# Performance work log

Hardware: AMD Instinct MI355X
Metric: run time of the kernel (lower is better)

The kernel has to match this reference:

```python
import jax, jax.numpy as jnp
import numpy as np

N_OBJ = 4096
IN_DIM = 1024
OUT_DIM = 1024
H = OUT_DIM // 2  # per-direction hidden, BidirectionalTreeLSTM uses out_dim//2
L = 2             # num_layer


def _build_tree(n):
    # balanced binary heap tree: node i has children 2i+1, 2i+2
    left = np.array([2 * i + 1 if 2 * i + 1 < n else -1 for i in range(n)], np.int32)
    right = np.array([2 * i + 2 if 2 * i + 2 < n else -1 for i in range(n)], np.int32)
    parent = np.full(n, -1, np.int32)
    for i in range(n):
        if left[i] >= 0:
            parent[left[i]] = i
        if right[i] >= 0:
            parent[right[i]] = i
    post, stack = [], [(0, False)]
    while stack:
        node, seen = stack.pop()
        if node < 0:
            continue
        if seen:
            post.append(node)
        else:
            stack.append((node, True))
            stack.append((int(right[node]), False))
            stack.append((int(left[node]), False))
    pre, stack = [], [0]
    while stack:
        node = stack.pop()
        if node < 0:
            continue
        pre.append(node)
        stack.append(int(right[node]))
        stack.append(int(left[node]))
    pad = lambda a: np.where(a < 0, n, a).astype(np.int32)  # slot n = zeros (no child/parent)
    return (np.array(post, np.int32), np.array(pre, np.int32),
            pad(left), pad(right), pad(parent))


def setup_inputs() -> dict:
    key = jax.random.key(0)
    ks = jax.random.split(key, 8)
    post, pre, left, right, parent = _build_tree(N_OBJ)

    def w(k, shape, fan_in):
        return jax.random.normal(k, shape, jnp.float32) * np.float32(1.0 / np.sqrt(fan_in))

    # bias init per the torch module: forget-gate blocks get constants, rest zero
    fw_bl = np.zeros((L, 6 * H), np.float32); fw_bl[:, 2 * H:4 * H] = 0.5
    fw_br = fw_bl.copy()
    bw_bh = np.zeros((L, 5 * H), np.float32); bw_bh[:, 2 * H:3 * H] = 1.0

    return {
        "features": jax.random.normal(ks[0], (N_OBJ, IN_DIM), jnp.float32),
        "fw_Wp": w(ks[1], (L, H, IN_DIM), IN_DIM),
        "fw_bp": jnp.zeros((L, H), jnp.float32),
        "fw_Wx": w(ks[2], (L, 6 * H, IN_DIM), IN_DIM),
        "fw_bx": jnp.zeros((L, 6 * H), jnp.float32),
        "fw_Wl": w(ks[3], (L, 6 * H, H), H),
        "fw_bl": jnp.asarray(fw_bl),
        "fw_Wr": w(ks[4], (L, 6 * H, H), H),
        "fw_br": jnp.asarray(fw_br),
        "bw_Wp": w(ks[5], (L, H, IN_DIM), IN_DIM),
        "bw_bp": jnp.zeros((L, H), jnp.float32),
        "bw_Wx": w(ks[6], (L, 5 * H, IN_DIM), IN_DIM),
        "bw_bx": jnp.zeros((L, 5 * H), jnp.float32),
        "bw_Wh": w(ks[7], (L, 5 * H, H), H),
        "bw_bh": jnp.asarray(bw_bh),
        "post_order": jnp.asarray(post),
        "pre_order": jnp.asarray(pre),
        "left_child": jnp.asarray(left),
        "right_child": jnp.asarray(right),
        "parent": jnp.asarray(parent),
    }


def _tree_leaves_to_root(feats, Wp, bp, Wx, bx, Wl, bl, Wr, br,
                         post_order, left_child, right_child):
    n = feats.shape[0]
    h = bp.shape[0]
    px = feats @ Wp.T + bp   # [n, h]   -- self path
    x2 = feats @ Wx.T + bx   # [n, 6h]  -- gate input, batched once

    def step(carry, idx):
        cbuf, hbuf = carry   # [n+1, h]; row n is permanent zero slot for missing children
        lc = left_child[idx]
        rc = right_child[idx]
        g = x2[idx] + hbuf[lc] @ Wl.T + bl + hbuf[rc] @ Wr.T + br
        i, o, fl, fr, u, r = jnp.split(g, 6)
        i = jax.nn.sigmoid(i); o = jax.nn.sigmoid(o)
        fl = jax.nn.sigmoid(fl); fr = jax.nn.sigmoid(fr)
        u = jnp.tanh(u); r = jax.nn.sigmoid(r)
        c = i * u + fl * cbuf[lc] + fr * cbuf[rc]
        hc = o * jnp.tanh(c)
        hf = r * hc + (1.0 - r) * px[idx]   # highway mix
        return (cbuf.at[idx].set(c), hbuf.at[idx].set(hf)), None

    init = (jnp.zeros((n + 1, h), feats.dtype), jnp.zeros((n + 1, h), feats.dtype))
    (_, hbuf), _ = jax.lax.scan(step, init, post_order)
    return hbuf[:n]


def _tree_root_to_leaves(feats, Wp, bp, Wx, bx, Wh, bh, pre_order, parent):
    n = feats.shape[0]
    h = bp.shape[0]
    px = feats @ Wp.T + bp   # [n, h]
    x2 = feats @ Wx.T + bx   # [n, 5h]

    def step(carry, idx):
        cbuf, hbuf = carry
        p = parent[idx]      # root maps to zero slot n -> iofuh(0) == bias, as in torch
        g = x2[idx] + hbuf[p] @ Wh.T + bh
        i, o, f, u, r = jnp.split(g, 5)
        i = jax.nn.sigmoid(i); o = jax.nn.sigmoid(o)
        f = jax.nn.sigmoid(f); u = jnp.tanh(u); r = jax.nn.sigmoid(r)
        c = i * u + f * cbuf[p]
        hc = o * jnp.tanh(c)
        hf = r * hc + (1.0 - r) * px[idx]
        return (cbuf.at[idx].set(c), hbuf.at[idx].set(hf)), None

    init = (jnp.zeros((n + 1, h), feats.dtype), jnp.zeros((n + 1, h), feats.dtype))
    (_, hbuf), _ = jax.lax.scan(step, init, pre_order)
    return hbuf[:n]


def reference(features, fw_Wp, fw_bp, fw_Wx, fw_bx, fw_Wl, fw_bl, fw_Wr, fw_br,
              bw_Wp, bw_bp, bw_Wx, bw_bx, bw_Wh, bw_bh,
              post_order, pre_order, left_child, right_child, parent):
    feats = features
    for l in range(L):  # MultiLayer_BTreeLSTM: stacked bidirectional layers
        h_fwd = _tree_leaves_to_root(feats, fw_Wp[l], fw_bp[l], fw_Wx[l], fw_bx[l],
                                     fw_Wl[l], fw_bl[l], fw_Wr[l], fw_br[l],
                                     post_order, left_child, right_child)
        h_bwd = _tree_root_to_leaves(feats, bw_Wp[l], bw_bp[l], bw_Wx[l], bw_bx[l],
                                     bw_Wh[l], bw_bh[l], pre_order, parent)
        feats = jnp.concatenate([h_fwd, h_bwd], axis=1)  # [n, out_dim]
    return feats
```

## Files before the change

kernel.cpp:

```cpp
#include <hip/hip_runtime.h>
#include <cstdint>
#include <cstddef>


#define HDIM 512
#define ZROW 4096
#define NCAT 6656

typedef _Float16 f16;
typedef f16   f16x8 __attribute__((ext_vector_type(8)));
typedef float f32x4 __attribute__((ext_vector_type(4)));

__device__ __forceinline__ float sigm(float x) { return 1.0f / (1.0f + expf(-x)); }

__device__ __forceinline__ void glds16(const f16* g, f16* l)
{
    __builtin_amdgcn_global_load_lds(
        (const __attribute__((address_space(1))) void*)g,
        (__attribute__((address_space(3))) void*)l,
        16, 0, 0);
}

#define VM4()   asm volatile("s_waitcnt vmcnt(4)" ::: "memory")
#define VM0()   asm volatile("s_waitcnt vmcnt(0)" ::: "memory")
#define BAR()   __builtin_amdgcn_s_barrier()
#define SP1()   __builtin_amdgcn_s_setprio(1)
#define SP0()   __builtin_amdgcn_s_setprio(0)

__device__ __forceinline__ void cvt8s(const float* __restrict__ s, f16* __restrict__ d)
{
    float4 v0 = ((const float4*)s)[0];
    float4 v1 = ((const float4*)s)[1];
    f16x8 o;
    o[0] = (f16)v0.x; o[1] = (f16)v0.y; o[2] = (f16)v0.z; o[3] = (f16)v0.w;
    o[4] = (f16)v1.x; o[5] = (f16)v1.y; o[6] = (f16)v1.z; o[7] = (f16)v1.w;
    *(f16x8*)d = o;
}

__global__ __launch_bounds__(256) void cvt16(
    const float* __restrict__ s, f16* __restrict__ d, int n8)
{
    int i = blockIdx.x * 256 + threadIdx.x;
    if (i >= n8) return;
    cvt8s(s + (size_t)i * 8, d + (size_t)i * 8);
}

__global__ __launch_bounds__(256) void prep_layer(
    const float* __restrict__ fWp, const float* __restrict__ fWx,
    const float* __restrict__ bWp, const float* __restrict__ bWx,
    const float* __restrict__ fWl, const float* __restrict__ fWr,
    const float* __restrict__ bWh,
    const float* __restrict__ fbp, const float* __restrict__ fbx,
    const float* __restrict__ bbp, const float* __restrict__ bbx,
    f16* __restrict__ Wcat, f16* __restrict__ Wlr, f16* __restrict__ Wh,
    float* __restrict__ biascat)
{
    const int bid = blockIdx.x;
    const int t   = threadIdx.x;
    if (bid < 256) {
        int i = bid * 256 + t;
        cvt8s(fWp + (size_t)i * 8, Wcat + (size_t)i * 8);
    } else if (bid < 1792) {
        int i = (bid - 256) * 256 + t;
        cvt8s(fWx + (size_t)i * 8, Wcat + (size_t)512 * 1024 + (size_t)i * 8);
    } else if (bid < 2048) {
        int i = (bid - 1792) * 256 + t;
        cvt8s(bWp + (size_t)i * 8, Wcat + (size_t)3584 * 1024 + (size_t)i * 8);
    } else if (bid < 3328) {
        int i = (bid - 2048) * 256 + t;
        cvt8s(bWx + (size_t)i * 8, Wcat + (size_t)4096 * 1024 + (size_t)i * 8);
    } else if (bid < 4864) {
        int i = (bid - 3328) * 256 + t;
        int col8 = (i * 8) & 1023;
        int row  = (i * 8) >> 10;
        const float* s = (col8 < HDIM) ? (fWl + (size_t)row * HDIM + col8)
                                       : (fWr + (size_t)row * HDIM + col8 - HDIM);
        int np = (row & 511) * 6 + (row >> 9);
        cvt8s(s, Wlr + (size_t)np * 1024 + col8);
    } else if (bid < 5504) {
        int i = (bid - 4864) * 256 + t;
        int col8 = (i * 8) & 511;
        int row  = (i * 8) >> 9;
        int np = (row & 511) * 5 + (row >> 9);
        cvt8s(bWh + (size_t)row * HDIM + col8, Wh + (size_t)np * HDIM + col8);
    } else {
        int i = (bid - 5504) * 256 + t;
        if (i >= NCAT) return;
        float v;
        if (i < 512) v = fbp[i];
        else if (i < 3584) v = fbx[i - 512];
        else if (i < 4096) v = bbp[i - 3584];
        else v = bbx[i - 4096];
        biascat[i] = v;
    }
}

__global__ void zero_slots(f16* H, float* cbf, float* cbb)
{
    int t = threadIdx.x;
    H[(size_t)ZROW * 1024 + t] = (f16)0.0f;
    if (t < HDIM) {
        cbf[(size_t)ZROW * HDIM + t] = 0.0f;
        cbb[(size_t)ZROW * HDIM + t] = 0.0f;
    }
}

__global__ __launch_bounds__(512) void mm_pre8(
    const f16* __restrict__ A, const f16* __restrict__ W,
    const float* __restrict__ bias, f16* __restrict__ C, int N, int K)
{
    __shared__ __align__(16) f16 lds[2][2][16384];
    const int t   = threadIdx.x;
    const int L   = t & 63;
    const int wid = t >> 6;
    const int wr  = wid >> 2;
    const int wc  = wid & 3;
    const int fr  = L & 15;
    const int fq  = L >> 4;
    const int srow = t >> 3;
    const int cs   = (((t & 7) ^ (srow & 7)) << 3);
    const int vrow = ((srow >> 5) << 6) + (srow & 31);
    const int bB0  = (srow >= 32) ? 2048 : 0;
    const f16* Ag = A + (size_t)(blockIdx.y * 256) * K + cs;
    const f16* Bg = W + (size_t)(blockIdx.x * 256) * K + cs;
    const int xa0 = ((fq)     ^ (fr & 7)) << 3;
    const int xa1 = ((4 + fq) ^ (fr & 7)) << 3;

#define STG_A(nb, T, u)                                                      \
    do {                                                                     \
        glds16(Ag + (size_t)(srow + (u) * 64) * K + (T) * 64,                \
               &lds[nb][0][(u) * 4096 + t * 8]);                             \
        glds16(Ag + (size_t)(srow + (u) * 64 + 128) * K + (T) * 64,          \
               &lds[nb][0][(u) * 4096 + 8192 + t * 8]);                      \
    } while (0)
#define STG_B(nb, T, v)                                                      \
    do {                                                                     \
        glds16(Bg + (size_t)(vrow + (v) * 32) * K + (T) * 64,                \
               &lds[nb][1][(v) * 2048 + bB0 + t * 8]);                       \
        glds16(Bg + (size_t)(vrow + (v) * 32 + 128) * K + (T) * 64,          \
               &lds[nb][1][(v) * 2048 + bB0 + 8192 + t * 8]);                \
    } while (0)

    f32x4 acc[8][4] = {};
    f16x8 a0f[4][2], a1f[4][2], b0f[2][2], b1f[2][2];

#define LDA(AF, Ar, mh)                                                            \
    do {                                                                           \
        _Pragma("unroll") for (int i2 = 0; i2 < 4; ++i2) {                         \
            AF[i2][0] = *(const f16x8*)((Ar) + ((mh) * 64 + i2 * 16) * 64 + xa0);  \
            AF[i2][1] = *(const f16x8*)((Ar) + ((mh) * 64 + i2 * 16) * 64 + xa1);  \
        }                                                                          \
    } while (0)
#define LDB(BF, Br, nh)                                                            \
    do {                                                                           \
        _Pragma("unroll") for (int j2 = 0; j2 < 2; ++j2) {                         \
            BF[j2][0] = *(const f16x8*)((Br) + ((nh) * 32 + j2 * 16) * 64 + xa0);  \
            BF[j2][1] = *(const f16x8*)((Br) + ((nh) * 32 + j2 * 16) * 64 + xa1);  \
        }                                                                          \
    } while (0)
#define MF(AF, BF, mh, nh)                                                         \
    do {                                                                           \
        _Pragma("unroll") for (int ks = 0; ks < 2; ++ks)                           \
        _Pragma("unroll") for (int i2 = 0; i2 < 4; ++i2)                           \
        _Pragma("unroll") for (int j2 = 0; j2 < 2; ++j2)                           \
            acc[(mh) * 4 + i2][(nh) * 2 + j2] =                                    \
                __builtin_amdgcn_mfma_f32_16x16x32_f16(                            \
                    AF[i2][ks], BF[j2][ks],                                        \
                    acc[(mh) * 4 + i2][(nh) * 2 + j2], 0, 0, 0);                   \
    } while (0)

    const int NT = K >> 6;
    STG_A(0, 0, 0); STG_B(0, 0, 0); STG_B(0, 0, 1); STG_A(0, 0, 1);
    VM0();
    BAR();

    for (int T = 0; T < NT; ++T) {
        const int cb = T & 1, nb = cb ^ 1;
        const bool pf = (T + 1 < NT);
        const f16* Ar = &lds[cb][0][(wr * 128 + fr) * 64];
        const f16* Br = &lds[cb][1][(wc * 64 + fr) * 64];
        LDA(a0f, Ar, 0); LDB(b0f, Br, 0);
        if (pf) STG_A(nb, T + 1, 0);
        VM4(); BAR();
        SP1(); MF(a0f, b0f, 0, 0); SP0();
        LDB(b1f, Br, 1);
        if (pf) STG_B(nb, T + 1, 0);
        VM4(); BAR();
        SP1(); MF(a0f, b1f, 0, 1); SP0();
        LDA(a1f, Ar, 1);
        if (pf) STG_B(nb, T + 1, 1);
        VM4(); BAR();
        SP1(); MF(a1f, b1f, 1, 1); SP0();
        if (pf) STG_A(nb, T + 1, 1);
        VM4(); BAR();
        SP1(); MF(a1f, b0f, 1, 0); SP0();
    }
#undef STG_A
#undef STG_B
#undef LDA
#undef LDB
#undef MF

    const int gr0 = blockIdx.y * 256 + wr * 128 + fq * 4;
    const int gc0 = blockIdx.x * 256 + wc * 64 + fr;
#pragma unroll
    for (int j = 0; j < 4; ++j) {
        const int gc = gc0 + j * 16;
        const float bj = bias[gc];
#pragma unroll
        for (int i = 0; i < 8; ++i) {
            const int gr = gr0 + i * 16;
#pragma unroll
            for (int rr = 0; rr < 4; ++rr)
                C[(size_t)(gr + rr) * N + gc] = (f16)(acc[i][j][rr] + bj);
        }
    }
}

__global__ __launch_bounds__(256) void stage_fused(
    const f16* __restrict__ Wlr, const f16* __restrict__ Wh,
    f16* H, const f16* __restrict__ PX,
    const int* __restrict__ lc, const int* __restrict__ rc,
    const int* __restrict__ par,
    int fbase, int fm, int bbase, int bm,
    float* __restrict__ cbf, float* __restrict__ cbb,
    float* out32,
    const float* __restrict__ bl, const float* __restrict__ br,
    const float* __restrict__ bh)
{
    __shared__ __align__(16) char smem[57344];
    f16*   Ab0 = (f16*)smem;
    f16*   Bb0 = (f16*)(smem + 32768);
    float* Sg  = (float*)smem;

    const int t   = threadIdx.x;
    const int L   = t & 63;
    const int w   = t >> 6;
    const int fr  = L & 15;
    const int fq  = L >> 4;
    const int rch = L >> 3;
    const int cs  = (((L & 7) ^ rch) << 3);
    const int fsw = (fr & 7) << 3;
    const int nfB = ((fm + 127) >> 7) * 32;

    if ((int)blockIdx.x < nfB) {
        const int by = blockIdx.x >> 5;
        const int bx = blockIdx.x & 31;
        const int wm = (w & 1) << 6;
        const int wn = (w >> 1) * 48;

        const f16* aLo[4]; const f16* aHi[4];
#pragma unroll
        for (int cc = 0; cc < 4; ++cc) {
            int g  = by * 128 + (w * 4 + cc) * 8 + rch;
            int n1 = ZROW, n2 = ZROW;
            if (g < fm) { n1 = lc[fbase + g]; n2 = rc[fbase + g]; }
            aLo[cc] = H + (size_t)n1 * 1024 + cs;
            aHi[cc] = H + (size_t)n2 * 1024 + cs - HDIM;
        }
        const f16* bsrc[3];
#pragma unroll
        for (int cc = 0; cc < 3; ++cc)
            bsrc[cc] = Wlr + (size_t)(bx * 96 + (w * 3 + cc) * 8 + rch) * 1024 + cs;

        f32x4 acc[4][3] = {};
#define STGF(sel, k0)                                                        \
        do {                                                                 \
            const bool hiK = (k0) >= HDIM;                                   \
            _Pragma("unroll")                                                \
            for (int cc = 0; cc < 4; ++cc)                                   \
                glds16((hiK ? aHi[cc] : aLo[cc]) + (k0),                     \
                       Ab0 + (sel) * 8192 + (w * 4 + cc) * 512 + L * 8);     \
            _Pragma("unroll")                                                \
            for (int cc = 0; cc < 3; ++cc)                                   \
                glds16(bsrc[cc] + (k0),                                      \
                       Bb0 + (sel) * 6144 + (w * 3 + cc) * 512 + L * 8);     \
        } while (0)

        STGF(0, 0);
        __syncthreads();
        int cur = 0;
        for (int tt = 0; tt < 16; ++tt) {
            if (tt + 1 < 16) STGF(cur ^ 1, (tt + 1) * 64);
            const f16* Ac = Ab0 + cur * 8192;
            const f16* Bc = Bb0 + cur * 6144;
            f16x8 af[4][2], bg[3][2];
#pragma unroll
            for (int i = 0; i < 4; ++i)
#pragma unroll
                for (int ks = 0; ks < 2; ++ks)
                    af[i][ks] = *(const f16x8*)(Ac + (wm + i * 16 + fr) * 64
                                + ((((ks * 4 + fq) << 3) ^ fsw)));
#pragma unroll
            for (int j = 0; j < 3; ++j)
#pragma unroll
                for (int ks = 0; ks < 2; ++ks)
                    bg[j][ks] = *(const f16x8*)(Bc + (wn + j * 16 + fr) * 64
                                + ((((ks * 4 + fq) << 3) ^ fsw)));
#pragma unroll
            for (int ks = 0; ks < 2; ++ks)
#pragma unroll
                for (int i = 0; i < 4; ++i)
#pragma unroll
                    for (int j = 0; j < 3; ++j)
                        acc[i][j] = __builtin_amdgcn_mfma_f32_16x16x32_f16(
                            af[i][ks], bg[j][ks], acc[i][j], 0, 0, 0);
            __syncthreads();
            cur ^= 1;
        }
#undef STGF
#pragma unroll
        for (int i = 0; i < 4; ++i)
#pragma unroll
            for (int j = 0; j < 3; ++j)
#pragma unroll
                for (int rr = 0; rr < 4; ++rr)
                    Sg[(wm + i * 16 + fq * 4 + rr) * 100 + wn + j * 16 + fr]
                        = acc[i][j][rr];
        __syncthreads();
        const int rmax = fm - by * 128;
        const int j0 = bx * 16;
        for (int cc = 0; cc < 8; ++cc) {
            int cell = t + cc * 256;
            int r = cell >> 4, j = cell & 15;
            if (r >= rmax) break;
            int node = fbase + by * 128 + r;
            int jj = j0 + j;
            const f16* pxr = PX + (size_t)node * NCAT;
            float g[6];
#pragma unroll
            for (int q = 0; q < 6; ++q)
                g[q] = (float)pxr[HDIM + q * HDIM + jj] + bl[q * HDIM + jj]
                     + br[q * HDIM + jj] + Sg[r * 100 + j * 6 + q];
            int lcn = lc[node], rcn = rc[node];
            float clv = cbf[(size_t)lcn * HDIM + jj];
            float crv = cbf[(size_t)rcn * HDIM + jj];
            float i_ = sigm(g[0]), o_ = sigm(g[1]), fl_ = sigm(g[2]), fr_ = sigm(g[3]);
            float u_ = tanhf(g[4]), r_ = sigm(g[5]);
            float c  = i_ * u_ + fl_ * clv + fr_ * crv;
            float hc = o_ * tanhf(c);
            float px = (float)pxr[jj];
            float hf = r_ * hc + (1.0f - r_) * px;
            cbf[(size_t)node * HDIM + jj] = c;
            H[(size_t)node * 1024 + jj] = (f16)hf;
            if (out32) out32[(size_t)node * 1024 + jj] = hf;
        }
    } else {
        const int b2 = blockIdx.x - nfB;
        const int by = b2 >> 5;
        const int bx = b2 & 31;
        const int wm = w * 32;

        const f16* asrc[4];
#pragma unroll
        for (int cc = 0; cc < 4; ++cc) {
            int g = by * 128 + (w * 4 + cc) * 8 + rch;
            int n1 = ZROW;
            if (g < bm) n1 = par[bbase + g];
            asrc[cc] = H + (size_t)n1 * 1024 + HDIM + cs;
        }
        const f16* bsrc[3];
        int nbch[3];
#pragma unroll
        for (int cc = 0; cc < 3; ++cc) {
            int ch = w * 3 + cc;
            nbch[cc] = ch;
            bsrc[cc] = Wh + (size_t)(bx * 80 + ch * 8 + rch) * HDIM + cs;
        }

        f32x4 acc[2][5] = {};
#define STGB(sel, k0)                                                        \
        do {                                                                 \
            _Pragma("unroll")                                                \
            for (int cc = 0; cc < 4; ++cc)                                   \
                glds16(asrc[cc] + (k0),                                      \
                       Ab0 + (sel) * 8192 + (w * 4 + cc) * 512 + L * 8);     \
            _Pragma("unroll")                                                \
            for (int cc = 0; cc < 3; ++cc)                                   \
                if (nbch[cc] < 10)                                           \
                    glds16(bsrc[cc] + (k0),                                  \
                           Bb0 + (sel) * 5120 + nbch[cc] * 512 + L * 8);     \
        } while (0)

        STGB(0, 0);
        __syncthreads();
        int cur = 0;
        for (int tt = 0; tt < 8; ++tt) {
            if (tt + 1 < 8) STGB(cur ^ 1, (tt + 1) * 64);
            const f16* Ac = Ab0 + cur * 8192;
            const f16* Bc = Bb0 + cur * 5120;
            f16x8 af[2][2], bg[5][2];
#pragma unroll
            for (int i = 0; i < 2; ++i)
#pragma unroll
                for (int ks = 0; ks < 2; ++ks)
                    af[i][ks] = *(const f16x8*)(Ac + (wm + i * 16 + fr) * 64
                                + ((((ks * 4 + fq) << 3) ^ fsw)));
#pragma unroll
            for (int j = 0; j < 5; ++j)
#pragma unroll
                for (int ks = 0; ks < 2; ++ks)
                    bg[j][ks] = *(const f16x8*)(Bc + ((j) * 16 + fr) * 64
                                + ((((ks * 4 + fq) << 3) ^ fsw)));
#pragma unroll
            for (int ks = 0; ks < 2; ++ks)
#pragma unroll
                for (int i = 0; i < 2; ++i)
#pragma unroll
                    for (int j = 0; j < 5; ++j)
                        acc[i][j] = __builtin_amdgcn_mfma_f32_16x16x32_f16(
                            af[i][ks], bg[j][ks], acc[i][j], 0, 0, 0);
            __syncthreads();
            cur ^= 1;
        }
#undef STGB
#pragma unroll
        for (int i = 0; i < 2; ++i)
#pragma unroll
            for (int j = 0; j < 5; ++j)
#pragma unroll
                for (int rr = 0; rr < 4; ++rr)
                    Sg[(wm + i * 16 + fq * 4 + rr) * 84 + j * 16 + fr]
                        = acc[i][j][rr];
        __syncthreads();
        const int rmax = bm - by * 128;
        const int j0 = bx * 16;
        for (int cc = 0; cc < 8; ++cc) {
            int cell = t + cc * 256;
            int r = cell >> 4, j = cell & 15;
            if (r >= rmax) break;
            int node = bbase + by * 128 + r;
            int jj = j0 + j;
            const f16* pxr = PX + (size_t)node * NCAT;
            float g[5];
#pragma unroll
            for (int q = 0; q < 5; ++q)
                g[q] = (float)pxr[4096 + q * HDIM + jj] + bh[q * HDIM + jj]
                     + Sg[r * 84 + j * 5 + q];
            int p = par[node];
            float cp = cbb[(size_t)p * HDIM + jj];
            float i_ = sigm(g[0]), o_ = sigm(g[1]), f_ = sigm(g[2]);
            float u_ = tanhf(g[3]), r_ = sigm(g[4]);
            float c  = i_ * u_ + f_ * cp;
            float hc = o_ * tanhf(c);
            float px = (float)pxr[3584 + jj];
            float hf = r_ * hc + (1.0f - r_) * px;
            cbb[(size_t)node * HDIM + jj] = c;
            H[(size_t)node * 1024 + HDIM + jj] = (f16)hf;
            if (out32) out32[(size_t)node * 1024 + HDIM + jj] = hf;
        }
    }
}

__global__ __launch_bounds__(256) void elem_merged(
    const f16* __restrict__ PX,
    int fbase, int fm, int bbase, int bm,
    const int* __restrict__ lc, const int* __restrict__ rc,
    const int* __restrict__ par,
    float* __restrict__ cbf, float* __restrict__ cbb,
    f16* __restrict__ H, float* __restrict__ out32,
    const float* __restrict__ bl, const float* __restrict__ br,
    const float* __restrict__ bh)
{
    int t = blockIdx.x * 256 + threadIdx.x;
    const int fvec = fm * 64;
    if (t < fvec) {
        int row = t >> 6, j8 = (t & 63) << 3;
        int node = fbase + row;
        const f16* pxr = PX + (size_t)node * NCAT;
        float g[6][8];
#pragma unroll
        for (int q = 0; q < 6; ++q) {
            f16x8 pv = *(const f16x8*)(pxr + HDIM + q * HDIM + j8);
            const float* blp = bl + q * HDIM + j8;
            const float* brp = br + q * HDIM + j8;
#pragma unroll
            for (int e = 0; e < 8; ++e)
                g[q][e] = (float)pv[e] + blp[e] + brp[e];
        }
        int lcn = lc[node], rcn = rc[node];
        const float* clp = cbf + (size_t)lcn * HDIM + j8;
        const float* crp = cbf + (size_t)rcn * HDIM + j8;
        f32x4 cl0 = *(const f32x4*)clp, cl1 = *(const f32x4*)(clp + 4);
        f32x4 cr0 = *(const f32x4*)crp, cr1 = *(const f32x4*)(crp + 4);
        f16x8 pxv = *(const f16x8*)(pxr + j8);
        f32x4 co0, co1;
        f16x8 hv;
        f32x4 ho0, ho1;
#pragma unroll
        for (int e = 0; e < 8; ++e) {
            float clv = (e < 4) ? cl0[e & 3] : cl1[e & 3];
            float crv = (e < 4) ? cr0[e & 3] : cr1[e & 3];
            float i_ = sigm(g[0][e]), o_ = sigm(g[1][e]);
            float fl_ = sigm(g[2][e]), fr_ = sigm(g[3][e]);
            float u_ = tanhf(g[4][e]), r_ = sigm(g[5][e]);
            float c  = i_ * u_ + fl_ * clv + fr_ * crv;
            float hc = o_ * tanhf(c);
            float hf = r_ * hc + (1.0f - r_) * (float)pxv[e];
            if (e < 4) { co0[e & 3] = c; ho0[e & 3] = hf; }
            else       { co1[e & 3] = c; ho1[e & 3] = hf; }
            hv[e] = (f16)hf;
        }
        float* cdst = cbf + (size_t)node * HDIM + j8;
        *(f32x4*)cdst = co0; *(f32x4*)(cdst + 4) = co1;
        *(f16x8*)(H + (size_t)node * 1024 + j8) = hv;
        if (out32) {
            float* od = out32 + (size_t)node * 1024 + j8;
            *(f32x4*)od = ho0; *(f32x4*)(od + 4) = ho1;
        }
    } else {
        int t2 = t - fvec;
        if (t2 >= bm * 64) return;
        int row = t2 >> 6, j8 = (t2 & 63) << 3;
        int node = bbase + row;
        const f16* pxr = PX + (size_t)node * NCAT;
        float g[5][8];
#pragma unroll
        for (int q = 0; q < 5; ++q) {
            f16x8 pv = *(const f16x8*)(pxr + 4096 + q * HDIM + j8);
            const float* bhp = bh + q * HDIM + j8;
#pragma unroll
            for (int e = 0; e < 8; ++e)
                g[q][e] = (float)pv[e] + bhp[e];
        }
        int p = par[node];
        const float* cpp = cbb + (size_t)p * HDIM + j8;
        f32x4 cp0 = *(const f32x4*)cpp, cp1 = *(const f32x4*)(cpp + 4);
        f16x8 pxv = *(const f16x8*)(pxr + 3584 + j8);
        f32x4 co0, co1;
        f16x8 hv;
        f32x4 ho0, ho1;
#pragma unroll
        for (int e = 0; e < 8; ++e) {
            float cpv = (e < 4) ? cp0[e & 3] : cp1[e & 3];
            float i_ = sigm(g[0][e]), o_ = sigm(g[1][e]), f_ = sigm(g[2][e]);
            float u_ = tanhf(g[3][e]), r_ = sigm(g[4][e]);
            float c  = i_ * u_ + f_ * cpv;
            float hc = o_ * tanhf(c);
            float hf = r_ * hc + (1.0f - r_) * (float)pxv[e];
            if (e < 4) { co0[e & 3] = c; ho0[e & 3] = hf; }
            else       { co1[e & 3] = c; ho1[e & 3] = hf; }
            hv[e] = (f16)hf;
        }
        float* cdst = cbb + (size_t)node * HDIM + j8;
        *(f32x4*)cdst = co0; *(f32x4*)(cdst + 4) = co1;
        *(f16x8*)(H + (size_t)node * 1024 + HDIM + j8) = hv;
        if (out32) {
            float* od = out32 + (size_t)node * 1024 + HDIM + j8;
            *(f32x4*)od = ho0; *(f32x4*)(od + 4) = ho1;
        }
    }
}

extern "C" void kernel_launch(void* const* d_in, const int* in_sizes, int n_in,
                              void* d_out, int out_size, void* d_ws, size_t ws_size,
                              hipStream_t stream)
{
    (void)in_sizes; (void)n_in; (void)out_size; (void)ws_size;
    const float* features = (const float*)d_in[0];
    const float* fw_Wp = (const float*)d_in[1];
    const float* fw_bp = (const float*)d_in[2];
    const float* fw_Wx = (const float*)d_in[3];
    const float* fw_bx = (const float*)d_in[4];
    const float* fw_Wl = (const float*)d_in[5];
    const float* fw_bl = (const float*)d_in[6];
    const float* fw_Wr = (const float*)d_in[7];
    const float* fw_br = (const float*)d_in[8];
    const float* bw_Wp = (const float*)d_in[9];
    const float* bw_bp = (const float*)d_in[10];
    const float* bw_Wx = (const float*)d_in[11];
    const float* bw_bx = (const float*)d_in[12];
    const float* bw_Wh = (const float*)d_in[13];
    const float* bw_bh = (const float*)d_in[14];
    const int* lc  = (const int*)d_in[17];
    const int* rc  = (const int*)d_in[18];
    const int* par = (const int*)d_in[19];

    f16* feat16 = (f16*)d_ws;
    f16* H      = feat16 + (size_t)4096 * 1024;
    f16* Wcat   = H     + (size_t)4097 * 1024;
    f16* Wlr    = Wcat  + (size_t)NCAT * 1024;
    f16* Wh     = Wlr   + (size_t)3072 * 1024;
    f16* PX     = Wh    + (size_t)2560 * 512;
    float* biascat = (float*)(PX + (size_t)4096 * NCAT);
    float* cbf     = biascat + NCAT;
    float* cbb     = cbf + (size_t)4097 * HDIM;

    zero_slots<<<dim3(1), dim3(1024), 0, stream>>>(H, cbf, cbb);
    cvt16<<<dim3(2048), 256, 0, stream>>>(features, feat16, 4096 * 1024 / 8);

    static const int fb[12] = {2047, 1023, 511, 255, 127, 63, 31, 15, 7, 3, 1, 0};
    static const int fmv[12] = {1, 1024, 512, 256, 128, 64, 32, 16, 8, 4, 2, 1};
    static const int bb[12] = {1, 3, 7, 15, 31, 63, 127, 255, 511, 1023, 2047, 4095};
    static const int bmv[12] = {2, 4, 8, 16, 32, 64, 128, 256, 512, 1024, 2048, 1};

    for (int l = 0; l < 2; ++l) {
        prep_layer<<<dim3(5530), 256, 0, stream>>>(
            fw_Wp + (size_t)l * 512 * 1024,  fw_Wx + (size_t)l * 3072 * 1024,
            bw_Wp + (size_t)l * 512 * 1024,  bw_Wx + (size_t)l * 2560 * 1024,
            fw_Wl + (size_t)l * 3072 * 512,  fw_Wr + (size_t)l * 3072 * 512,
            bw_Wh + (size_t)l * 2560 * 512,
            fw_bp + (size_t)l * 512, fw_bx + (size_t)l * 3072,
            bw_bp + (size_t)l * 512, bw_bx + (size_t)l * 2560,
            Wcat, Wlr, Wh, biascat);

        const f16* A16 = (l == 0) ? feat16 : H;
        mm_pre8<<<dim3(NCAT / 256, 4096 / 256), 512, 0, stream>>>(
            A16, Wcat, biascat, PX, NCAT, 1024);

        float* o32 = (l == 1) ? (float*)d_out : nullptr;
        const float* bl_l = fw_bl + (size_t)l * 3072;
        const float* br_l = fw_br + (size_t)l * 3072;
        const float* bh_l = bw_bh + (size_t)l * 2560;

        {
            int tot = (2048 + 1) * 64;
            elem_merged<<<dim3((tot + 255) / 256), 256, 0, stream>>>(
                PX, 2048, 2048, 0, 1,
                lc, rc, par, cbf, cbb, H, o32, bl_l, br_l, bh_l);
        }
        for (int i = 0; i < 12; ++i) {
            int nfB = ((fmv[i] + 127) >> 7) * 32;
            int nbB = ((bmv[i] + 127) >> 7) * 32;
            stage_fused<<<dim3(nfB + nbB), 256, 0, stream>>>(
                Wlr, Wh, H, PX, lc, rc, par,
                fb[i], fmv[i], bb[i], bmv[i],
                cbf, cbb, o32, bl_l, br_l, bh_l);
        }
    }
}
```

Measured before the change: 777.5 us.

## Deepen stage_fused K-loop to four LDS buffers with prefetch distance two

New measurement: 751.7 us. 3.3% less time.

```diff
diff --git a/kernel.cpp b/kernel.cpp
--- a/kernel.cpp
+++ b/kernel.cpp
@@ -21,9 +21,12 @@
         16, 0, 0);
 }
 
+#define VM7()   asm volatile("s_waitcnt vmcnt(7)" ::: "memory")
+#define VM5()   asm volatile("s_waitcnt vmcnt(5)" ::: "memory")
 #define VM4()   asm volatile("s_waitcnt vmcnt(4)" ::: "memory")
 #define VM0()   asm volatile("s_waitcnt vmcnt(0)" ::: "memory")
-#define BAR()   __builtin_amdgcn_s_barrier()
+#define BAR()   do { __builtin_amdgcn_s_barrier(); \
+                     __builtin_amdgcn_sched_barrier(0); } while (0)
 #define SP1()   __builtin_amdgcn_s_setprio(1)
 #define SP0()   __builtin_amdgcn_s_setprio(0)
 
@@ -228,9 +231,9 @@
     const float* __restrict__ bl, const float* __restrict__ br,
     const float* __restrict__ bh)
 {
-    __shared__ __align__(16) char smem[57344];
+    __shared__ __align__(16) char smem[114688];
     f16*   Ab0 = (f16*)smem;
-    f16*   Bb0 = (f16*)(smem + 32768);
+    f16*   Bb0 = (f16*)(smem + 65536);
     float* Sg  = (float*)smem;
 
     const int t   = threadIdx.x;
@@ -264,26 +267,24 @@
             bsrc[cc] = Wlr + (size_t)(bx * 96 + (w * 3 + cc) * 8 + rch) * 1024 + cs;
 
         f32x4 acc[4][3] = {};
-#define STGF(sel, k0)                                                        \
+#define STGF(b, k0)                                                          \
         do {                                                                 \
             const bool hiK = (k0) >= HDIM;                                   \
             _Pragma("unroll")                                                \
             for (int cc = 0; cc < 4; ++cc)                                   \
                 glds16((hiK ? aHi[cc] : aLo[cc]) + (k0),                     \
-                       Ab0 + (sel) * 8192 + (w * 4 + cc) * 512 + L * 8);     \
+                       Ab0 + (b) * 8192 + (w * 4 + cc) * 512 + L * 8);       \
             _Pragma("unroll")                                                \
             for (int cc = 0; cc < 3; ++cc)                                   \
                 glds16(bsrc[cc] + (k0),                                      \
-                       Bb0 + (sel) * 6144 + (w * 3 + cc) * 512 + L * 8);     \
+                       Bb0 + (b) * 6144 + (w * 3 + cc) * 512 + L * 8);       \
         } while (0)
 
-        STGF(0, 0);
-        __syncthreads();
-        int cur = 0;
+        STGF(0, 0); STGF(1, 64);
+        VM7(); BAR();
         for (int tt = 0; tt < 16; ++tt) {
-            if (tt + 1 < 16) STGF(cur ^ 1, (tt + 1) * 64);
-            const f16* Ac = Ab0 + cur * 8192;
-            const f16* Bc = Bb0 + cur * 6144;
+            const f16* Ac = Ab0 + (tt & 3) * 8192;
+            const f16* Bc = Bb0 + (tt & 3) * 6144;
             f16x8 af[4][2], bg[3][2];
 #pragma unroll
             for (int i = 0; i < 4; ++i)
@@ -297,6 +298,9 @@
                 for (int ks = 0; ks < 2; ++ks)
                     bg[j][ks] = *(const f16x8*)(Bc + (wn + j * 16 + fr) * 64
                                 + ((((ks * 4 + fq) << 3) ^ fsw)));
+            if (tt + 2 < 16) { STGF((tt + 2) & 3, (tt + 2) * 64); VM7(); }
+            else if (tt + 1 < 16) VM0();
+            BAR();
 #pragma unroll
             for (int ks = 0; ks < 2; ++ks)
 #pragma unroll
@@ -305,10 +309,9 @@
                     for (int j = 0; j < 3; ++j)
                         acc[i][j] = __builtin_amdgcn_mfma_f32_16x16x32_f16(
                             af[i][ks], bg[j][ks], acc[i][j], 0, 0, 0);
-            __syncthreads();
-            cur ^= 1;
         }
 #undef STGF
+        __syncthreads();
 #pragma unroll
         for (int i = 0; i < 4; ++i)
 #pragma unroll
@@ -369,26 +372,25 @@
         }
 
         f32x4 acc[2][5] = {};
-#define STGB(sel, k0)                                                        \
+#define STGB(b, k0)                                                          \
         do {                                                                 \
             _Pragma("unroll")                                                \
             for (int cc = 0; cc < 4; ++cc)                                   \
                 glds16(asrc[cc] + (k0),                                      \
-                       Ab0 + (sel) * 8192 + (w * 4 + cc) * 512 + L * 8);     \
+                       Ab0 + (b) * 8192 + (w * 4 + cc) * 512 + L * 8);       \
             _Pragma("unroll")                                                \
             for (int cc = 0; cc < 3; ++cc)                                   \
                 if (nbch[cc] < 10)                                           \
                     glds16(bsrc[cc] + (k0),                                  \
-                           Bb0 + (sel) * 5120 + nbch[cc] * 512 + L * 8);     \
+                           Bb0 + (b) * 5120 + nbch[cc] * 512 + L * 8);       \
         } while (0)
-
-        STGB(0, 0);
-        __syncthreads();
-        int cur = 0;
+#define VMB()   do { if (w == 3) { VM5(); } else { VM7(); } } while (0)
+
+        STGB(0, 0); STGB(1, 64);
+        VMB(); BAR();
         for (int tt = 0; tt < 8; ++tt) {
-            if (tt + 1 < 8) STGB(cur ^ 1, (tt + 1) * 64);
-            const f16* Ac = Ab0 + cur * 8192;
-            const f16* Bc = Bb0 + cur * 5120;
+            const f16* Ac = Ab0 + (tt & 3) * 8192;
+            const f16* Bc = Bb0 + (tt & 3) * 5120;
             f16x8 af[2][2], bg[5][2];
 #pragma unroll
             for (int i = 0; i < 2; ++i)
@@ -402,6 +404,9 @@
                 for (int ks = 0; ks < 2; ++ks)
                     bg[j][ks] = *(const f16x8*)(Bc + ((j) * 16 + fr) * 64
                                 + ((((ks * 4 + fq) << 3) ^ fsw)));
+            if (tt + 2 < 8) { STGB((tt + 2) & 3, (tt + 2) * 64); VMB(); }
+            else if (tt + 1 < 8) VM0();
+            BAR();
 #pragma unroll
             for (int ks = 0; ks < 2; ++ks)
 #pragma unroll
@@ -410,10 +415,10 @@
                     for (int j = 0; j < 5; ++j)
                         acc[i][j] = __builtin_amdgcn_mfma_f32_16x16x32_f16(
                             af[i][ks], bg[j][ks], acc[i][j], 0, 0, 0);
-            __syncthreads();
-            cur ^= 1;
         }
 #undef STGB
+#undef VMB
+        __syncthreads();
 #pragma unroll
         for (int i = 0; i < 2; ++i)
 #pragma unroll
```
